# Kernel optimization log

Measured on AMD Instinct MI355X. Metric: run time of the kernel, lower is better.

Reference implementation:

```python
import jax, jax.numpy as jnp
import numpy as np

PAD = 0
EPS = 1e-5


def setup_inputs() -> dict:
    key = jax.random.key(0)
    k1, k2, k3, k4, k5 = jax.random.split(key, 5)
    B, S, D, H = 16, 1024, 512, 4
    output = jax.random.normal(k1, (B, S, D), dtype=jnp.float32)
    local_cor = jax.random.normal(k2, (1,), dtype=jnp.float32)
    event_type = jax.random.randint(k3, (B, S), 0, 1000, dtype=jnp.int64)
    # xavier-ish scale for the per-layer Linear weights
    W = jax.random.normal(k4, (H, D, D), dtype=jnp.float32) * (1.0 / np.sqrt(D))
    b = jax.random.normal(k5, (H, D), dtype=jnp.float32) * 0.01
    return {"output": output, "local_cor": local_cor, "event_type": event_type, "W": W, "b": b}


def _build_mask(event_type, S, dtype):
    # subsequent mask: 1 for strictly-future positions (triu, diag=1)
    subseq = jnp.triu(jnp.ones((S, S), dtype=dtype), k=1)  # [S,S]
    # key-pad mask: 1 where key token is PAD, broadcast over query dim
    keypad = (event_type == PAD).astype(dtype)[:, None, :]  # [B,1,S]
    return ((keypad + subseq[None]) > 0).astype(dtype)  # [B,S,S]


def reference(output, local_cor, event_type, W, b):
    B, S, D = output.shape
    H = W.shape[0]
    temperature = jnp.asarray(D, output.dtype) ** 0.5
    mask = _build_mask(event_type, S, output.dtype)  # [B,S,S]

    x = output
    total = None
    for h in range(H):  # heads are applied SEQUENTIALLY in the original
        # masked QK^T scores
        attn = jnp.einsum('bqd,bkd->bqk', x / temperature, x) * mask  # [B,S,S]
        # L2 normalize along keys (F.normalize p=2, eps=1e-5)
        norm = jnp.sqrt(jnp.sum(attn * attn, axis=-1, keepdims=True))
        attn = attn / jnp.maximum(norm, EPS)
        # value path: ELU(Linear(x))
        v = jax.nn.elu(jnp.einsum('bsd,ed->bse', x, W[h]) + b[h])  # [B,S,D]
        x = jnp.einsum('bqk,bkd->bqd', attn, v)
        total = x if total is None else total + x
    return total
```

## Files before the change

### kernel.cpp

```cpp
#include <hip/hip_runtime.h>
#include <math.h>

#define B_ 16
#define S_ 1024
#define D_ 512
#define H_ 4
#define INV_TEMP 0.044194173824159216f
#define C_SCALE 0.00390625f
#define OUT_SCALE 256.0f

typedef _Float16 f16;
typedef _Float16 f16x8 __attribute__((ext_vector_type(8)));
typedef _Float16 f16x4 __attribute__((ext_vector_type(4)));
typedef float f32x4 __attribute__((ext_vector_type(4)));

#define AS1(p) ((const __attribute__((address_space(1))) void*)(p))
#define AS3(p) ((__attribute__((address_space(3))) void*)(p))
#define MFMA __builtin_amdgcn_mfma_f32_16x16x32_f16

__global__ __launch_bounds__(256)
void k_conv(const float* __restrict__ src, f16* __restrict__ dst)
{
    const int i = blockIdx.x * 256 + threadIdx.x;
    const float4 v = ((const float4*)src)[i];
    f16x4 h; h[0] = (f16)v.x; h[1] = (f16)v.y; h[2] = (f16)v.z; h[3] = (f16)v.w;
    ((f16x4*)dst)[i] = h;
}

__global__ __launch_bounds__(128)
void k_flags(const int* __restrict__ etype, int* __restrict__ flag)
{
    const int t = threadIdx.x;
    const int b = t >> 3, kt = t & 7;
    const int* p = etype + b * S_ + kt * 128;
    int any0 = 0;
#pragma unroll
    for (int i = 0; i < 128; i += 4) {
        const int4 v = *(const int4*)(p + i);
        any0 |= (v.x == 0) | (v.y == 0) | (v.z == 0) | (v.w == 0);
    }
    flag[t] = any0;
}

__device__ __forceinline__ void stage128x32(const f16* __restrict__ src, int ld,
                                            char* lds0, int t)
{
    const f16* g0 = src + (size_t)(t >> 2) * ld + (t & 3) * 8;
    __builtin_amdgcn_global_load_lds(AS1(g0), AS3(lds0 + t * 16), 16, 0, 0);
    const f16* g1 = g0 + (size_t)64 * ld;
    __builtin_amdgcn_global_load_lds(AS1(g1), AS3(lds0 + 4096 + t * 16), 16, 0, 0);
}

__device__ __forceinline__ void mma_chunk(const char* ldsA, const char* ldsB,
                                          int wm, int wn, int lr, int quad,
                                          f32x4 (*acc)[4])
{
    f16x8 af[4], bf[4];
#pragma unroll
    for (int i = 0; i < 4; ++i)
        af[i] = *(const f16x8*)(ldsA + ((wm * 64 + i * 16 + lr) * 32 + quad * 8) * 2);
#pragma unroll
    for (int j = 0; j < 4; ++j)
        bf[j] = *(const f16x8*)(ldsB + ((wn * 64 + j * 16 + lr) * 32 + quad * 8) * 2);
#pragma unroll
    for (int i = 0; i < 4; ++i)
#pragma unroll
        for (int j = 0; j < 4; ++j)
            acc[i][j] = MFMA(af[i], bf[j], acc[i][j], 0, 0, 0);
}

__device__ __forceinline__ void gemm_core(const f16* A, int ldA, const f16* Bm, int ldB,
                                          int K, char* lds, int t, int wm, int wn,
                                          int lr, int quad, f32x4 (*acc)[4])
{
    for (int k0 = 0; k0 < K; k0 += 32) {
        stage128x32(A + k0, ldA, lds, t);
        stage128x32(Bm + k0, ldB, lds + 8192, t);
        __syncthreads();
        mma_chunk(lds, lds + 8192, wm, wn, lr, quad, acc);
        __syncthreads();
    }
}

__global__ __launch_bounds__(256)
void k_vs(const f16* __restrict__ xh, const f16* __restrict__ Wh,
          const float* __restrict__ bias, f16* __restrict__ vT,
          const int* __restrict__ etype, const int* __restrict__ flag,
          f16* __restrict__ sh, float* __restrict__ ss)
{
    __shared__ __align__(16) char lds[16384];
    const int t = threadIdx.x;
    const int w = t >> 6, lane = t & 63, lr = lane & 15, quad = lane >> 4;
    const int wm = w & 1, wn = w >> 1;

    if (blockIdx.x < 1024) {
        const int i0 = blockIdx.x;
        const int xcd = i0 & 7, j0 = i0 >> 3;
        const int b = 2 * xcd + (j0 & 1);
        const int tile = j0 >> 1;
        const int bk = (tile & 7) * 128;
        const int bq = (tile >> 3) * 128;
        if (bk < bq && !flag[b * 8 + (bk >> 7)]) return;

        const f16* xb = xh + (size_t)b * S_ * D_;
        f32x4 acc[4][4] = {};
        gemm_core(xb + (size_t)bk * D_, D_, xb + (size_t)bq * D_, D_, D_,
                  lds, t, wm, wn, lr, quad, acc);
        const float sc = INV_TEMP * C_SCALE;
        float ssq[4] = {0.0f, 0.0f, 0.0f, 0.0f};
#pragma unroll
        for (int i = 0; i < 4; ++i) {
            const int k4 = bk + wm * 64 + i * 16 + quad * 4;
            const int4 et = *(const int4*)(etype + b * S_ + k4);
            const int ev[4] = {et.x, et.y, et.z, et.w};
#pragma unroll
            for (int j = 0; j < 4; ++j) {
                const int q = bq + wn * 64 + j * 16 + lr;
                f16x4 hv;
#pragma unroll
                for (int r = 0; r < 4; ++r) {
                    const bool keep = ((k4 + r) > q) || (ev[r] == 0);
                    hv[r] = (f16)(keep ? acc[i][j][r] * sc : 0.0f);
                    const float fv = (float)hv[r];
                    ssq[j] += fv * fv;
                }
                *(f16x4*)(sh + ((size_t)b * S_ + q) * S_ + k4) = hv;
            }
        }
#pragma unroll
        for (int j = 0; j < 4; ++j) {
            float v = ssq[j];
            v += __shfl_xor(v, 16, 64);
            v += __shfl_xor(v, 32, 64);
            if (quad == 0) {
                const int q = bq + wn * 64 + j * 16 + lr;
                atomicAdd(ss + b * S_ + q, v);
            }
        }
    } else {
        const int idx = blockIdx.x - 1024;
        const int bm = (idx & 127) * 128;
        const int bn = (idx >> 7) * 128;
        f32x4 acc[4][4] = {};
        gemm_core(xh + (size_t)bm * D_, D_, Wh + (size_t)bn * D_, D_, D_,
                  lds, t, wm, wn, lr, quad, acc);
#pragma unroll
        for (int j = 0; j < 4; ++j) {
            const int e = bn + wn * 64 + j * 16 + lr;
            const float be = bias[e];
#pragma unroll
            for (int i = 0; i < 4; ++i) {
                const int m = bm + wm * 64 + i * 16 + quad * 4;
                const int batch = m >> 10, s = m & 1023;
                f16x4 hv;
#pragma unroll
                for (int r = 0; r < 4; ++r) {
                    float z = acc[i][j][r] + be;
                    z = (z > 0.0f) ? z : (expf(z) - 1.0f);
                    hv[r] = (f16)z;
                }
                *(f16x4*)(vT + ((size_t)batch * D_ + e) * S_ + s) = hv;
            }
        }
    }
}

__global__ __launch_bounds__(256)
void k_out(const f16* __restrict__ vT, const f16* __restrict__ sh,
           const float* __restrict__ ss, const int* __restrict__ flag,
           f16* __restrict__ xh, float* __restrict__ out, const int accum)
{
    __shared__ __align__(16) char lds[16384];
    const int t = threadIdx.x;
    const int w = t >> 6, lane = t & 63, lr = lane & 15, quad = lane >> 4;
    const int wm = w & 1, wn = w >> 1;
    const int i0 = blockIdx.x;
    const int xcd = i0 & 7, j0 = i0 >> 3;
    const int b = 2 * xcd + (j0 & 1);
    const int tile = j0 >> 1;
    const int be = (tile & 3) * 128;
    const int bq = (tile >> 2) * 128;
    const int qt = bq >> 7;

    const f16* Abase = vT + ((size_t)b * D_ + be) * S_;
    const f16* Bbase = sh + ((size_t)b * S_ + bq) * S_;
    f32x4 acc[4][4] = {};
#pragma unroll 1
    for (int kt = 0; kt < 8; ++kt) {
        if (kt < qt && !flag[b * 8 + kt]) continue;
        const int kb = kt * 128;
        for (int k0 = kb; k0 < kb + 128; k0 += 32) {
            stage128x32(Abase + k0, S_, lds, t);
            stage128x32(Bbase + k0, S_, lds + 8192, t);
            __syncthreads();
            mma_chunk(lds, lds + 8192, wm, wn, lr, quad, acc);
            __syncthreads();
        }
    }
#pragma unroll
    for (int j = 0; j < 4; ++j) {
        const int q = bq + wn * 64 + j * 16 + lr;
        const float ssv = ss[b * S_ + q];
        const float scl = 1.0f / (C_SCALE * fmaxf(sqrtf(ssv) * OUT_SCALE, 1e-5f));
#pragma unroll
        for (int i = 0; i < 4; ++i) {
            const int e4 = be + wm * 64 + i * 16 + quad * 4;
            const size_t o = ((size_t)b * S_ + q) * D_ + e4;
            f32x4 xnew;
            f16x4 hx;
#pragma unroll
            for (int r = 0; r < 4; ++r) {
                xnew[r] = acc[i][j][r] * scl;
                hx[r] = (f16)xnew[r];
            }
            f32x4 val = xnew;
            if (accum) { const f32x4 old = *(const f32x4*)(out + o); val = val + old; }
            *(f32x4*)(out + o) = val;
            *(f16x4*)(xh + o) = hx;
        }
    }
}

extern "C" void kernel_launch(void* const* d_in, const int* in_sizes, int n_in,
                              void* d_out, int out_size, void* d_ws, size_t ws_size,
                              hipStream_t stream) {
    const float* x0    = (const float*)d_in[0];
    const int*   etype = (const int*)d_in[2];
    const float* W     = (const float*)d_in[3];
    const float* bias  = (const float*)d_in[4];
    float* out = (float*)d_out;

    char* ws = (char*)d_ws;
    f16*   xh    = (f16*)(ws);
    f16*   vT    = (f16*)(ws + (16u << 20));
    f16*   sh    = (f16*)(ws + (32u << 20));
    f16*   Wh    = (f16*)(ws + (64u << 20));
    float* ssb   = (float*)(ws + (66u << 20));
    int*   flags = (int*)(ws + (66u << 20) + 262144);

    k_conv <<<8192, 256, 0, stream>>>(x0, xh);
    k_conv <<<1024, 256, 0, stream>>>(W, Wh);
    k_flags<<<1, 128, 0, stream>>>(etype, flags);
    hipMemsetAsync(sh, 0, (size_t)32 << 20, stream);
    hipMemsetAsync(ssb, 0, 4 * (size_t)B_ * S_ * sizeof(float), stream);

    for (int h = 0; h < H_; ++h) {
        float* ss = ssb + (size_t)h * B_ * S_;
        k_vs <<<1536, 256, 0, stream>>>(xh, Wh + (size_t)h * D_ * D_,
                                        bias + (size_t)h * D_, vT,
                                        etype, flags, sh, ss);
        k_out<<<512, 256, 0, stream>>>(vT, sh, ss, flags, xh, out, h > 0);
    }
}
```

Baseline: 371.6 us.

## Double-buffer LDS staging in GEMM loops to overlap loads with MFMA

Replaces the single-buffer stage/sync/compute/sync loop with a ping-pong LDS scheme: the next K-chunk is staged into the alternate buffer while MFMAs run on the current one, which removes one barrier per iteration. In the output kernel, the list of active K-chunks (after skipping masked tiles) is built once into shared memory so the pipelined loop can iterate over it. LDS usage doubles to 32 KB per block, which may reduce occupancy, and stage128x32 may be a synchronous global-to-LDS copy, in which case there is little real overlap.

```diff
diff --git a/kernel.cpp b/kernel.cpp
--- a/kernel.cpp
+++ b/kernel.cpp
@@ -69,17 +69,55 @@
             acc[i][j] = MFMA(af[i], bf[j], acc[i][j], 0, 0, 0);
 }
 
-__device__ __forceinline__ void gemm_core(const f16* A, int ldA, const f16* Bm, int ldB,
-                                          int K, char* lds, int t, int wm, int wn,
-                                          int lr, int quad, f32x4 (*acc)[4])
-{
-    for (int k0 = 0; k0 < K; k0 += 32) {
+__device__ __forceinline__ void gemm_db(const f16* __restrict__ A, int ldA,
+                                        const f16* __restrict__ Bm, int ldB,
+                                        int K, char* lds, int t, int wm, int wn,
+                                        int lr, int quad, f32x4 (*acc)[4])
+{
+    stage128x32(A, ldA, lds, t);
+    stage128x32(Bm, ldB, lds + 8192, t);
+    __syncthreads();
+    int cur = 0;
+#pragma unroll 1
+    for (int k0 = 32; k0 < K; k0 += 32) {
+        char* nxt = lds + ((cur ^ 1) << 14);
+        stage128x32(A + k0, ldA, nxt, t);
+        stage128x32(Bm + k0, ldB, nxt + 8192, t);
+        char* c = lds + (cur << 14);
+        mma_chunk(c, c + 8192, wm, wn, lr, quad, acc);
+        __syncthreads();
+        cur ^= 1;
+    }
+    char* c = lds + (cur << 14);
+    mma_chunk(c, c + 8192, wm, wn, lr, quad, acc);
+}
+
+__device__ __forceinline__ void gemm_db_list(const f16* __restrict__ A, int ldA,
+                                             const f16* __restrict__ Bm, int ldB,
+                                             const int* __restrict__ klist, int nst,
+                                             char* lds, int t, int wm, int wn,
+                                             int lr, int quad, f32x4 (*acc)[4])
+{
+    {
+        const int k0 = klist[0];
         stage128x32(A + k0, ldA, lds, t);
         stage128x32(Bm + k0, ldB, lds + 8192, t);
+    }
+    __syncthreads();
+    int cur = 0;
+#pragma unroll 1
+    for (int i = 1; i < nst; ++i) {
+        const int k0 = klist[i];
+        char* nxt = lds + ((cur ^ 1) << 14);
+        stage128x32(A + k0, ldA, nxt, t);
+        stage128x32(Bm + k0, ldB, nxt + 8192, t);
+        char* c = lds + (cur << 14);
+        mma_chunk(c, c + 8192, wm, wn, lr, quad, acc);
         __syncthreads();
-        mma_chunk(lds, lds + 8192, wm, wn, lr, quad, acc);
-        __syncthreads();
-    }
+        cur ^= 1;
+    }
+    char* c = lds + (cur << 14);
+    mma_chunk(c, c + 8192, wm, wn, lr, quad, acc);
 }
 
 __global__ __launch_bounds__(256)
@@ -88,7 +126,7 @@
           const int* __restrict__ etype, const int* __restrict__ flag,
           f16* __restrict__ sh, float* __restrict__ ss)
 {
-    __shared__ __align__(16) char lds[16384];
+    __shared__ __align__(16) char lds[32768];
     const int t = threadIdx.x;
     const int w = t >> 6, lane = t & 63, lr = lane & 15, quad = lane >> 4;
     const int wm = w & 1, wn = w >> 1;
@@ -104,8 +142,8 @@
 
         const f16* xb = xh + (size_t)b * S_ * D_;
         f32x4 acc[4][4] = {};
-        gemm_core(xb + (size_t)bk * D_, D_, xb + (size_t)bq * D_, D_, D_,
-                  lds, t, wm, wn, lr, quad, acc);
+        gemm_db(xb + (size_t)bk * D_, D_, xb + (size_t)bq * D_, D_, D_,
+                lds, t, wm, wn, lr, quad, acc);
         const float sc = INV_TEMP * C_SCALE;
         float ssq[4] = {0.0f, 0.0f, 0.0f, 0.0f};
 #pragma unroll
@@ -142,8 +180,8 @@
         const int bm = (idx & 127) * 128;
         const int bn = (idx >> 7) * 128;
         f32x4 acc[4][4] = {};
-        gemm_core(xh + (size_t)bm * D_, D_, Wh + (size_t)bn * D_, D_, D_,
-                  lds, t, wm, wn, lr, quad, acc);
+        gemm_db(xh + (size_t)bm * D_, D_, Wh + (size_t)bn * D_, D_, D_,
+                lds, t, wm, wn, lr, quad, acc);
 #pragma unroll
         for (int j = 0; j < 4; ++j) {
             const int e = bn + wn * 64 + j * 16 + lr;
@@ -170,7 +208,9 @@
            const float* __restrict__ ss, const int* __restrict__ flag,
            f16* __restrict__ xh, float* __restrict__ out, const int accum)
 {
-    __shared__ __align__(16) char lds[16384];
+    __shared__ __align__(16) char lds[32768];
+    __shared__ int klist[32];
+    __shared__ int kcnt;
     const int t = threadIdx.x;
     const int w = t >> 6, lane = t & 63, lr = lane & 15, quad = lane >> 4;
     const int wm = w & 1, wn = w >> 1;
@@ -182,21 +222,27 @@
     const int bq = (tile >> 2) * 128;
     const int qt = bq >> 7;
 
-    const f16* Abase = vT + ((size_t)b * D_ + be) * S_;
-    const f16* Bbase = sh + ((size_t)b * S_ + bq) * S_;
+    if (t == 0) {
+        int n = 0;
+        for (int kc = 0; kc < 8; ++kc)
+            if (kc >= qt || flag[b * 8 + kc]) {
+                const int kb = kc * 128;
+                klist[n]     = kb;
+                klist[n + 1] = kb + 32;
+                klist[n + 2] = kb + 64;
+                klist[n + 3] = kb + 96;
+                n += 4;
+            }
+        kcnt = n;
+    }
+    __syncthreads();
+    const int nst = kcnt;
+
     f32x4 acc[4][4] = {};
-#pragma unroll 1
-    for (int kt = 0; kt < 8; ++kt) {
-        if (kt < qt && !flag[b * 8 + kt]) continue;
-        const int kb = kt * 128;
-        for (int k0 = kb; k0 < kb + 128; k0 += 32) {
-            stage128x32(Abase + k0, S_, lds, t);
-            stage128x32(Bbase + k0, S_, lds + 8192, t);
-            __syncthreads();
-            mma_chunk(lds, lds + 8192, wm, wn, lr, quad, acc);
-            __syncthreads();
-        }
-    }
+    gemm_db_list(vT + ((size_t)b * D_ + be) * S_, S_,
+                 sh + ((size_t)b * S_ + bq) * S_, S_,
+                 klist, nst, lds, t, wm, wn, lr, quad, acc);
+
 #pragma unroll
     for (int j = 0; j < 4; ++j) {
         const int q = bq + wn * 64 + j * 16 + lr;
```

Result: slower. 404.1 us (+8.7%).

## Rewrite score/value GEMM as 256x256 tiles with pipelined swizzled LDS staging

Applied to the files above, without the earlier changes.

k_vs now uses 512-thread blocks computing 256x256 output tiles with a hand-scheduled, software-pipelined K loop. Staging is double-buffered and XOR-swizzled in 128 KB of LDS, with explicit waitcnt, sched barriers and setprio around the MFMA bursts. The goal is to hide global load latency, raise MFMA utilisation, and cut the number of blocks and redundant staging compared with the 128x128 single-buffer loop. k_out also precomputes the list of non-skipped K chunks and stops writing the fp16 x copy on the last head. The large LDS footprint allows only one block per CU, and the coarser tiles skip fewer masked tiles.

```diff
diff --git a/kernel.cpp b/kernel.cpp
--- a/kernel.cpp
+++ b/kernel.cpp
@@ -18,6 +18,20 @@
 #define AS3(p) ((__attribute__((address_space(3))) void*)(p))
 #define MFMA __builtin_amdgcn_mfma_f32_16x16x32_f16
 
+#define SBAR()                                                                 \
+    do {                                                                       \
+        __builtin_amdgcn_sched_barrier(0);                                     \
+        __builtin_amdgcn_s_barrier();                                          \
+        __builtin_amdgcn_sched_barrier(0);                                     \
+    } while (0)
+
+#define VMF(N)                                                                 \
+    do {                                                                       \
+        __builtin_amdgcn_sched_barrier(0);                                     \
+        asm volatile("s_waitcnt vmcnt(" #N ")" ::: "memory");                  \
+        __builtin_amdgcn_sched_barrier(0);                                     \
+    } while (0)
+
 __global__ __launch_bounds__(256)
 void k_conv(const float* __restrict__ src, f16* __restrict__ dst)
 {
@@ -42,6 +56,188 @@
     flag[t] = any0;
 }
 
+__device__ __forceinline__ void stage_half(const f16* __restrict__ mat, int ld,
+                                           int koff, int rowbase,
+                                           char* lds, int dstbase, int t)
+{
+    const int r = rowbase + (t >> 3);
+    const int c = ((t & 7) ^ ((t >> 3) & 7)) << 3;
+    const f16* g0 = mat + (size_t)r * ld + koff + c;
+    __builtin_amdgcn_global_load_lds(AS1(g0), AS3(lds + dstbase + t * 16), 16, 0, 0);
+    const f16* g1 = g0 + (size_t)64 * ld;
+    __builtin_amdgcn_global_load_lds(AS1(g1), AS3(lds + dstbase + 8192 + t * 16), 16, 0, 0);
+}
+
+#define PHASE(P, ABASE, BBASE, FENCE, ...)                                     \
+    {                                                                          \
+        f16x8 ar[2][2];                                                        \
+        if ((P) == 0) {                                                        \
+            _Pragma("unroll") for (int nj_ = 0; nj_ < 4; ++nj_)                \
+                _Pragma("unroll") for (int kk_ = 0; kk_ < 2; ++kk_)            \
+                    br[nj_][kk_] =                                             \
+                        *(const f16x8*)(lds + (BBASE) + offB[nj_][kk_]);       \
+        }                                                                      \
+        _Pragma("unroll") for (int f_ = 0; f_ < 2; ++f_)                       \
+            _Pragma("unroll") for (int kk_ = 0; kk_ < 2; ++kk_)                \
+                ar[f_][kk_] =                                                  \
+                    *(const f16x8*)(lds + (ABASE) + offA[2 * (P) + f_][kk_]);  \
+        __VA_ARGS__;                                                           \
+        SBAR();                                                                \
+        asm volatile("s_waitcnt lgkmcnt(0)" ::: "memory");                     \
+        __builtin_amdgcn_sched_barrier(0);                                     \
+        __builtin_amdgcn_s_setprio(1);                                         \
+        _Pragma("unroll") for (int f_ = 0; f_ < 2; ++f_)                       \
+            _Pragma("unroll") for (int nj_ = 0; nj_ < 4; ++nj_)                \
+                _Pragma("unroll") for (int kk_ = 0; kk_ < 2; ++kk_)            \
+                    acc[2 * (P) + f_][nj_] = MFMA(ar[f_][kk_], br[nj_][kk_],   \
+                                                  acc[2 * (P) + f_][nj_],      \
+                                                  0, 0, 0);                    \
+        __builtin_amdgcn_s_setprio(0);                                         \
+        FENCE;                                                                 \
+        SBAR();                                                                \
+    }
+
+__device__ __forceinline__ void gemm256_k512(const f16* __restrict__ A, int ldA,
+                                             const f16* __restrict__ Bm, int ldB,
+                                             char* lds, int t, f32x4 (*acc)[4])
+{
+    const int lane = t & 63, lr = lane & 15, quad = lane >> 4;
+    const int w = t >> 6, wm = w >> 2, wn = w & 3;
+
+    int offA[8][2], offB[4][2];
+#pragma unroll
+    for (int fi = 0; fi < 8; ++fi) {
+        const int row = wm * 128 + fi * 16 + lr;
+#pragma unroll
+        for (int kk = 0; kk < 2; ++kk)
+            offA[fi][kk] = row * 128 + ((((kk << 2) + quad) ^ (row & 7)) << 4);
+    }
+#pragma unroll
+    for (int nj = 0; nj < 4; ++nj) {
+        const int row = wn * 64 + nj * 16 + lr;
+#pragma unroll
+        for (int kk = 0; kk < 2; ++kk)
+            offB[nj][kk] = row * 128 + ((((kk << 2) + quad) ^ (row & 7)) << 4);
+    }
+
+    f16x8 br[4][2];
+
+    stage_half(A,  ldA, 0,  0,   lds, 0,      t);
+    stage_half(A,  ldA, 0,  128, lds, 16384,  t);
+    stage_half(Bm, ldB, 0,  0,   lds, 32768,  t);
+    stage_half(Bm, ldB, 0,  128, lds, 49152,  t);
+    stage_half(Bm, ldB, 64, 0,   lds, 98304,  t);
+    stage_half(Bm, ldB, 64, 128, lds, 114688, t);
+    VMF(4);
+    SBAR();
+
+#pragma unroll 1
+    for (int it = 0; it < 3; ++it) {
+        const int ko1 = it * 128 + 64, ko2 = it * 128 + 128, ko3 = it * 128 + 192;
+        PHASE(0, 0, 32768, (void)0, stage_half(A, ldA, ko1, 0,   lds, 65536, t))
+        PHASE(1, 0, 32768, (void)0, stage_half(A, ldA, ko1, 128, lds, 81920, t))
+        PHASE(2, 0, 32768, (void)0, stage_half(Bm, ldB, ko2, 0,   lds, 32768, t))
+        PHASE(3, 0, 32768, VMF(4),  stage_half(Bm, ldB, ko2, 128, lds, 49152, t))
+        PHASE(0, 65536, 98304, (void)0, stage_half(A, ldA, ko2, 0,   lds, 0,      t))
+        PHASE(1, 65536, 98304, (void)0, stage_half(A, ldA, ko2, 128, lds, 16384,  t))
+        PHASE(2, 65536, 98304, (void)0, stage_half(Bm, ldB, ko3, 0,   lds, 98304,  t))
+        PHASE(3, 65536, 98304, VMF(4),  stage_half(Bm, ldB, ko3, 128, lds, 114688, t))
+    }
+    PHASE(0, 0, 32768, (void)0, stage_half(A, ldA, 448, 0,   lds, 65536, t))
+    PHASE(1, 0, 32768, (void)0, stage_half(A, ldA, 448, 128, lds, 81920, t))
+    PHASE(2, 0, 32768, (void)0, (void)0)
+    PHASE(3, 0, 32768, VMF(0),  (void)0)
+    PHASE(0, 65536, 98304, (void)0, (void)0)
+    PHASE(1, 65536, 98304, (void)0, (void)0)
+    PHASE(2, 65536, 98304, (void)0, (void)0)
+    PHASE(3, 65536, 98304, (void)0, (void)0)
+}
+
+__global__ __launch_bounds__(512)
+void k_vs(const f16* __restrict__ xh, const f16* __restrict__ Wh,
+          const float* __restrict__ bias, f16* __restrict__ vT,
+          const int* __restrict__ etype, const int* __restrict__ flag,
+          f16* __restrict__ sh, float* __restrict__ ss)
+{
+    __shared__ __align__(16) char lds[131072];
+    const int t = threadIdx.x;
+    const int lane = t & 63, lr = lane & 15, quad = lane >> 4;
+    const int w = t >> 6, wm = w >> 2, wn = w & 3;
+
+    if (blockIdx.x < 256) {
+        const int i0 = blockIdx.x;
+        const int xcd = i0 & 7, j0 = i0 >> 3;
+        const int b = 2 * xcd + (j0 & 1);
+        const int tile = j0 >> 1;
+        const int kt2 = tile & 3, qt2 = tile >> 2;
+        if (kt2 < qt2 && !(flag[b * 8 + 2 * kt2] | flag[b * 8 + 2 * kt2 + 1]))
+            return;
+        const int bk = kt2 * 256, bq = qt2 * 256;
+        const f16* xb = xh + (size_t)b * S_ * D_;
+        f32x4 acc[8][4] = {};
+        gemm256_k512(xb + (size_t)bk * D_, D_, xb + (size_t)bq * D_, D_,
+                     lds, t, acc);
+        const float sc = INV_TEMP * C_SCALE;
+        float ssq[4] = {0.f, 0.f, 0.f, 0.f};
+#pragma unroll
+        for (int fi = 0; fi < 8; ++fi) {
+            const int k4 = bk + wm * 128 + fi * 16 + quad * 4;
+            const int4 et = *(const int4*)(etype + b * S_ + k4);
+            const int ev[4] = {et.x, et.y, et.z, et.w};
+#pragma unroll
+            for (int nj = 0; nj < 4; ++nj) {
+                const int q = bq + wn * 64 + nj * 16 + lr;
+                f16x4 hv;
+#pragma unroll
+                for (int r = 0; r < 4; ++r) {
+                    const bool keep = ((k4 + r) > q) || (ev[r] == 0);
+                    hv[r] = (f16)(keep ? acc[fi][nj][r] * sc : 0.0f);
+                    const float fv = (float)hv[r];
+                    ssq[nj] += fv * fv;
+                }
+                *(f16x4*)(sh + ((size_t)b * S_ + q) * S_ + k4) = hv;
+            }
+        }
+#pragma unroll
+        for (int nj = 0; nj < 4; ++nj) {
+            float v = ssq[nj];
+            v += __shfl_xor(v, 16, 64);
+            v += __shfl_xor(v, 32, 64);
+            if (quad == 0)
+                atomicAdd(ss + b * S_ + (bq + wn * 64 + nj * 16 + lr), v);
+        }
+    } else {
+        const int idx = blockIdx.x - 256;
+        const int xcd = idx & 7, j = idx >> 3;
+        const int b = 2 * xcd + (j & 1);
+        const int rest = j >> 1;
+        const int sq = rest & 3, bnT = rest >> 2;
+        const int bm = b * 1024 + sq * 256;
+        const int bn = bnT * 256;
+        f32x4 acc[8][4] = {};
+        gemm256_k512(xh + (size_t)bm * D_, D_, Wh + (size_t)bn * D_, D_,
+                     lds, t, acc);
+#pragma unroll
+        for (int nj = 0; nj < 4; ++nj) {
+            const int e = bn + wn * 64 + nj * 16 + lr;
+            const float be = bias[e];
+#pragma unroll
+            for (int fi = 0; fi < 8; ++fi) {
+                const int m = bm + wm * 128 + fi * 16 + quad * 4;
+                const int s = m & 1023;
+                f16x4 hv;
+#pragma unroll
+                for (int r = 0; r < 4; ++r) {
+                    float z = acc[fi][nj][r] + be;
+                    z = (z > 0.0f) ? z : (expf(z) - 1.0f);
+                    hv[r] = (f16)z;
+                }
+                *(f16x4*)(vT + ((size_t)b * D_ + e) * S_ + s) = hv;
+            }
+        }
+    }
+}
+
 __device__ __forceinline__ void stage128x32(const f16* __restrict__ src, int ld,
                                             char* lds0, int t)
 {
@@ -69,108 +265,15 @@
             acc[i][j] = MFMA(af[i], bf[j], acc[i][j], 0, 0, 0);
 }
 
-__device__ __forceinline__ void gemm_core(const f16* A, int ldA, const f16* Bm, int ldB,
-                                          int K, char* lds, int t, int wm, int wn,
-                                          int lr, int quad, f32x4 (*acc)[4])
-{
-    for (int k0 = 0; k0 < K; k0 += 32) {
-        stage128x32(A + k0, ldA, lds, t);
-        stage128x32(Bm + k0, ldB, lds + 8192, t);
-        __syncthreads();
-        mma_chunk(lds, lds + 8192, wm, wn, lr, quad, acc);
-        __syncthreads();
-    }
-}
-
-__global__ __launch_bounds__(256)
-void k_vs(const f16* __restrict__ xh, const f16* __restrict__ Wh,
-          const float* __restrict__ bias, f16* __restrict__ vT,
-          const int* __restrict__ etype, const int* __restrict__ flag,
-          f16* __restrict__ sh, float* __restrict__ ss)
-{
-    __shared__ __align__(16) char lds[16384];
-    const int t = threadIdx.x;
-    const int w = t >> 6, lane = t & 63, lr = lane & 15, quad = lane >> 4;
-    const int wm = w & 1, wn = w >> 1;
-
-    if (blockIdx.x < 1024) {
-        const int i0 = blockIdx.x;
-        const int xcd = i0 & 7, j0 = i0 >> 3;
-        const int b = 2 * xcd + (j0 & 1);
-        const int tile = j0 >> 1;
-        const int bk = (tile & 7) * 128;
-        const int bq = (tile >> 3) * 128;
-        if (bk < bq && !flag[b * 8 + (bk >> 7)]) return;
-
-        const f16* xb = xh + (size_t)b * S_ * D_;
-        f32x4 acc[4][4] = {};
-        gemm_core(xb + (size_t)bk * D_, D_, xb + (size_t)bq * D_, D_, D_,
-                  lds, t, wm, wn, lr, quad, acc);
-        const float sc = INV_TEMP * C_SCALE;
-        float ssq[4] = {0.0f, 0.0f, 0.0f, 0.0f};
-#pragma unroll
-        for (int i = 0; i < 4; ++i) {
-            const int k4 = bk + wm * 64 + i * 16 + quad * 4;
-            const int4 et = *(const int4*)(etype + b * S_ + k4);
-            const int ev[4] = {et.x, et.y, et.z, et.w};
-#pragma unroll
-            for (int j = 0; j < 4; ++j) {
-                const int q = bq + wn * 64 + j * 16 + lr;
-                f16x4 hv;
-#pragma unroll
-                for (int r = 0; r < 4; ++r) {
-                    const bool keep = ((k4 + r) > q) || (ev[r] == 0);
-                    hv[r] = (f16)(keep ? acc[i][j][r] * sc : 0.0f);
-                    const float fv = (float)hv[r];
-                    ssq[j] += fv * fv;
-                }
-                *(f16x4*)(sh + ((size_t)b * S_ + q) * S_ + k4) = hv;
-            }
-        }
-#pragma unroll
-        for (int j = 0; j < 4; ++j) {
-            float v = ssq[j];
-            v += __shfl_xor(v, 16, 64);
-            v += __shfl_xor(v, 32, 64);
-            if (quad == 0) {
-                const int q = bq + wn * 64 + j * 16 + lr;
-                atomicAdd(ss + b * S_ + q, v);
-            }
-        }
-    } else {
-        const int idx = blockIdx.x - 1024;
-        const int bm = (idx & 127) * 128;
-        const int bn = (idx >> 7) * 128;
-        f32x4 acc[4][4] = {};
-        gemm_core(xh + (size_t)bm * D_, D_, Wh + (size_t)bn * D_, D_, D_,
-                  lds, t, wm, wn, lr, quad, acc);
-#pragma unroll
-        for (int j = 0; j < 4; ++j) {
-            const int e = bn + wn * 64 + j * 16 + lr;
-            const float be = bias[e];
-#pragma unroll
-            for (int i = 0; i < 4; ++i) {
-                const int m = bm + wm * 64 + i * 16 + quad * 4;
-                const int batch = m >> 10, s = m & 1023;
-                f16x4 hv;
-#pragma unroll
-                for (int r = 0; r < 4; ++r) {
-                    float z = acc[i][j][r] + be;
-                    z = (z > 0.0f) ? z : (expf(z) - 1.0f);
-                    hv[r] = (f16)z;
-                }
-                *(f16x4*)(vT + ((size_t)batch * D_ + e) * S_ + s) = hv;
-            }
-        }
-    }
-}
-
 __global__ __launch_bounds__(256)
 void k_out(const f16* __restrict__ vT, const f16* __restrict__ sh,
            const float* __restrict__ ss, const int* __restrict__ flag,
-           f16* __restrict__ xh, float* __restrict__ out, const int accum)
+           f16* __restrict__ xh, float* __restrict__ out,
+           const int accum, const int wxh)
 {
     __shared__ __align__(16) char lds[16384];
+    __shared__ int klist[32];
+    __shared__ int kcnt;
     const int t = threadIdx.x;
     const int w = t >> 6, lane = t & 63, lr = lane & 15, quad = lane >> 4;
     const int wm = w & 1, wn = w >> 1;
@@ -182,21 +285,33 @@
     const int bq = (tile >> 2) * 128;
     const int qt = bq >> 7;
 
+    if (t == 0) {
+        int n = 0;
+        for (int kc = 0; kc < 8; ++kc)
+            if (kc >= qt || flag[b * 8 + kc]) {
+                const int kb = kc * 128;
+                klist[n] = kb; klist[n + 1] = kb + 32;
+                klist[n + 2] = kb + 64; klist[n + 3] = kb + 96;
+                n += 4;
+            }
+        kcnt = n;
+    }
+    __syncthreads();
+    const int nst = kcnt;
+
     const f16* Abase = vT + ((size_t)b * D_ + be) * S_;
     const f16* Bbase = sh + ((size_t)b * S_ + bq) * S_;
     f32x4 acc[4][4] = {};
 #pragma unroll 1
-    for (int kt = 0; kt < 8; ++kt) {
-        if (kt < qt && !flag[b * 8 + kt]) continue;
-        const int kb = kt * 128;
-        for (int k0 = kb; k0 < kb + 128; k0 += 32) {
-            stage128x32(Abase + k0, S_, lds, t);
-            stage128x32(Bbase + k0, S_, lds + 8192, t);
-            __syncthreads();
-            mma_chunk(lds, lds + 8192, wm, wn, lr, quad, acc);
-            __syncthreads();
-        }
-    }
+    for (int i = 0; i < nst; ++i) {
+        const int k0 = klist[i];
+        stage128x32(Abase + k0, S_, lds, t);
+        stage128x32(Bbase + k0, S_, lds + 8192, t);
+        __syncthreads();
+        mma_chunk(lds, lds + 8192, wm, wn, lr, quad, acc);
+        __syncthreads();
+    }
+
 #pragma unroll
     for (int j = 0; j < 4; ++j) {
         const int q = bq + wn * 64 + j * 16 + lr;
@@ -216,7 +331,7 @@
             f32x4 val = xnew;
             if (accum) { const f32x4 old = *(const f32x4*)(out + o); val = val + old; }
             *(f32x4*)(out + o) = val;
-            *(f16x4*)(xh + o) = hx;
+            if (wxh) *(f16x4*)(xh + o) = hx;
         }
     }
 }
@@ -246,9 +361,10 @@
 
     for (int h = 0; h < H_; ++h) {
         float* ss = ssb + (size_t)h * B_ * S_;
-        k_vs <<<1536, 256, 0, stream>>>(xh, Wh + (size_t)h * D_ * D_,
-                                        bias + (size_t)h * D_, vT,
-                                        etype, flags, sh, ss);
-        k_out<<<512, 256, 0, stream>>>(vT, sh, ss, flags, xh, out, h > 0);
-    }
-}
+        k_vs <<<384, 512, 0, stream>>>(xh, Wh + (size_t)h * D_ * D_,
+                                       bias + (size_t)h * D_, vT,
+                                       etype, flags, sh, ss);
+        k_out<<<512, 256, 0, stream>>>(vT, sh, ss, flags, xh, out,
+                                       h > 0, h < H_ - 1);
+    }
+}
```

Result: slower. 417.8 us (+12.4%).

## Split k_out K-loop across two 256-thread groups with LDS reduction

Applied to the files above, without the earlier changes.

Doubles the k_out block to 512 threads and splits the list of non-skipped K chunks between two independent 256-thread groups, each with its own LDS staging buffer. The partial accumulators are then reduced through LDS before the epilogue. This targets low occupancy with only 512 blocks on a large-CU device, and also skips writing the fp16 x copy on the last head. The costs are larger LDS use per block, an extra reduction pass, and block-wide barriers shared by both groups.

```diff
diff --git a/kernel.cpp b/kernel.cpp
--- a/kernel.cpp
+++ b/kernel.cpp
@@ -165,14 +165,19 @@
     }
 }
 
-__global__ __launch_bounds__(256)
+__global__ __launch_bounds__(512)
 void k_out(const f16* __restrict__ vT, const f16* __restrict__ sh,
            const float* __restrict__ ss, const int* __restrict__ flag,
-           f16* __restrict__ xh, float* __restrict__ out, const int accum)
-{
-    __shared__ __align__(16) char lds[16384];
+           f16* __restrict__ xh, float* __restrict__ out,
+           const int accum, const int wxh)
+{
+    __shared__ __align__(16) char lds[65536];
+    __shared__ int klist[32];
+    __shared__ int kcnt;
     const int t = threadIdx.x;
-    const int w = t >> 6, lane = t & 63, lr = lane & 15, quad = lane >> 4;
+    const int g = t >> 8;
+    const int tl = t & 255;
+    const int w = tl >> 6, lane = tl & 63, lr = lane & 15, quad = lane >> 4;
     const int wm = w & 1, wn = w >> 1;
     const int i0 = blockIdx.x;
     const int xcd = i0 & 7, j0 = i0 >> 3;
@@ -182,41 +187,68 @@
     const int bq = (tile >> 2) * 128;
     const int qt = bq >> 7;
 
+    if (t == 0) {
+        int n = 0;
+        for (int kc = 0; kc < 8; ++kc)
+            if (kc >= qt || flag[b * 8 + kc]) {
+                const int kb = kc * 128;
+                klist[n] = kb; klist[n + 1] = kb + 32;
+                klist[n + 2] = kb + 64; klist[n + 3] = kb + 96;
+                n += 4;
+            }
+        kcnt = n;
+    }
+    __syncthreads();
+    const int half = kcnt >> 1;
+    const int s0 = g ? half : 0;
+
     const f16* Abase = vT + ((size_t)b * D_ + be) * S_;
     const f16* Bbase = sh + ((size_t)b * S_ + bq) * S_;
+    char* myl = lds + (g << 14);
     f32x4 acc[4][4] = {};
 #pragma unroll 1
-    for (int kt = 0; kt < 8; ++kt) {
-        if (kt < qt && !flag[b * 8 + kt]) continue;
-        const int kb = kt * 128;
-        for (int k0 = kb; k0 < kb + 128; k0 += 32) {
-            stage128x32(Abase + k0, S_, lds, t);
-            stage128x32(Bbase + k0, S_, lds + 8192, t);
-            __syncthreads();
-            mma_chunk(lds, lds + 8192, wm, wn, lr, quad, acc);
-            __syncthreads();
-        }
-    }
-#pragma unroll
-    for (int j = 0; j < 4; ++j) {
-        const int q = bq + wn * 64 + j * 16 + lr;
-        const float ssv = ss[b * S_ + q];
-        const float scl = 1.0f / (C_SCALE * fmaxf(sqrtf(ssv) * OUT_SCALE, 1e-5f));
-#pragma unroll
-        for (int i = 0; i < 4; ++i) {
-            const int e4 = be + wm * 64 + i * 16 + quad * 4;
-            const size_t o = ((size_t)b * S_ + q) * D_ + e4;
-            f32x4 xnew;
-            f16x4 hx;
-#pragma unroll
-            for (int r = 0; r < 4; ++r) {
-                xnew[r] = acc[i][j][r] * scl;
-                hx[r] = (f16)xnew[r];
-            }
-            f32x4 val = xnew;
-            if (accum) { const f32x4 old = *(const f32x4*)(out + o); val = val + old; }
-            *(f32x4*)(out + o) = val;
-            *(f16x4*)(xh + o) = hx;
+    for (int i = 0; i < half; ++i) {
+        const int k0 = klist[s0 + i];
+        stage128x32(Abase + k0, S_, myl, tl);
+        stage128x32(Bbase + k0, S_, myl + 8192, tl);
+        __syncthreads();
+        mma_chunk(myl, myl + 8192, wm, wn, lr, quad, acc);
+        __syncthreads();
+    }
+
+    if (g == 1) {
+#pragma unroll
+        for (int j = 0; j < 4; ++j)
+#pragma unroll
+            for (int i = 0; i < 4; ++i)
+                *(f32x4*)(lds + (((w * 16 + j * 4 + i) * 64 + lane) << 4)) = acc[i][j];
+    }
+    __syncthreads();
+    if (g == 0) {
+#pragma unroll
+        for (int j = 0; j < 4; ++j) {
+            const int q = bq + wn * 64 + j * 16 + lr;
+            const float ssv = ss[b * S_ + q];
+            const float scl = 1.0f / (C_SCALE * fmaxf(sqrtf(ssv) * OUT_SCALE, 1e-5f));
+#pragma unroll
+            for (int i = 0; i < 4; ++i) {
+                const f32x4 other =
+                    *(const f32x4*)(lds + (((w * 16 + j * 4 + i) * 64 + lane) << 4));
+                const f32x4 sum = acc[i][j] + other;
+                const int e4 = be + wm * 64 + i * 16 + quad * 4;
+                const size_t o = ((size_t)b * S_ + q) * D_ + e4;
+                f32x4 xnew;
+                f16x4 hx;
+#pragma unroll
+                for (int r = 0; r < 4; ++r) {
+                    xnew[r] = sum[r] * scl;
+                    hx[r] = (f16)xnew[r];
+                }
+                f32x4 val = xnew;
+                if (accum) { const f32x4 old = *(const f32x4*)(out + o); val = val + old; }
+                *(f32x4*)(out + o) = val;
+                if (wxh) *(f16x4*)(xh + o) = hx;
+            }
         }
     }
 }
@@ -249,6 +281,7 @@
         k_vs <<<1536, 256, 0, stream>>>(xh, Wh + (size_t)h * D_ * D_,
                                         bias + (size_t)h * D_, vT,
                                         etype, flags, sh, ss);
-        k_out<<<512, 256, 0, stream>>>(vT, sh, ss, flags, xh, out, h > 0);
-    }
-}
+        k_out<<<512, 512, 0, stream>>>(vT, sh, ss, flags, xh, out,
+                                       h > 0, h < H_ - 1);
+    }
+}
```

Result: faster. 363.4 us (-2.2%).
